# Kernel tuning notes

Hardware: AMD Instinct MI355X
Metric: run time of the kernel (lower is better)

## Reference

```python
import jax, jax.numpy as jnp
import numpy as np


def setup_inputs() -> dict:
    key = jax.random.key(0)
    ks = jax.random.split(key, 5)
    B, H, W, KV = 32, 32, 32, 1024
    N, K, V = 16, 64, 64
    return {
        "key_value": jax.random.normal(ks[0], (B, H, W, KV), dtype=jnp.float32),
        "query": jax.random.normal(ks[1], (1, 1, N, K), dtype=jnp.float32),
        "k_kernel": jax.random.normal(ks[2], (KV, N * K), dtype=jnp.float32) * 0.03,
        "k_bias": jnp.zeros((N * K,), dtype=jnp.float32),
        "v_kernel": jax.random.normal(ks[3], (KV, N * V), dtype=jnp.float32) * 0.03,
        "v_bias": jnp.zeros((N * V,), dtype=jnp.float32),
    }


def reference(key_value, query, k_kernel, k_bias, v_kernel, v_bias):
    # key_value: [B,H,W,KV]; 1x1 conv == channel GEMM
    B, H, W, KV = key_value.shape
    N, K = query.shape[2], query.shape[3]
    V = v_kernel.shape[1] // N
    x = key_value.reshape(B, H * W, KV)                      # [B,HW,KV]
    k = (x @ k_kernel + k_bias).reshape(B, H * W, N, K)       # [B,HW,N,K]
    v = (x @ v_kernel + v_bias).reshape(B, H * W, N, V)       # [B,HW,N,V]
    # single-query dot product per head (no 1/sqrt(K) scaling, per original)
    logits = jnp.einsum('bsnk,nk->bsn', k, query[0, 0])       # [B,HW,N]
    attn = jax.nn.softmax(logits, axis=1)                     # softmax over HW
    out = jnp.einsum('bsn,bsnv->bnv', attn, v)                # [B,N,V]
    return out
```

## Files before the change

### kernel.cpp

```cpp
#include <hip/hip_runtime.h>
#include <hip/hip_fp16.h>


__device__ __forceinline__ float rlane(float v, int l) {
  return __int_as_float(__builtin_amdgcn_readlane(__float_as_int(v), l));
}

__global__ __launch_bounds__(256) void k_qk(const float* __restrict__ kk,
                                            const float* __restrict__ q,
                                            const float* __restrict__ kb,
                                            float* __restrict__ qk2,
                                            float* __restrict__ qb) {
  const int gid = blockIdx.x * 256 + threadIdx.x;
  const int c = gid >> 4, n = gid & 15;
  float a = 0.f;
#pragma unroll
  for (int k4 = 0; k4 < 64; k4 += 4) {
    const float4 kv = *(const float4*)(kk + (size_t)c * 1024 + n * 64 + k4);
    const float4 qv = *(const float4*)(q + n * 64 + k4);
    a += kv.x * qv.x + kv.y * qv.y + kv.z * qv.z + kv.w * qv.w;
  }
  qk2[(n >> 2) * 4096 + c * 4 + (n & 3)] = a;
  if (blockIdx.x == 0 && threadIdx.x < 16) {
    float s = 0.f;
    for (int k = 0; k < 64; k++) s += kb[threadIdx.x * 64 + k] * q[threadIdx.x * 64 + k];
    qb[threadIdx.x] = s;
  }
}

__global__ __launch_bounds__(512, 4) void k_fused(const float* __restrict__ x,
                                                  const float* __restrict__ qk2,
                                                  const float* __restrict__ qb,
                                                  float* __restrict__ mch,
                                                  float* __restrict__ lch,
                                                  __half* __restrict__ wph) {
  __shared__ float qkt[16384];
  __shared__ float et2[64 * 17 + 4];
  const int tid = threadIdx.x;
  const int lane = tid & 63;
  const int wid = tid >> 6;
  const int blk = blockIdx.x;
  const int srow0 = blk * 64;

#pragma unroll
  for (int it = 0; it < 8; ++it) {
    const int g = it * 512 + tid;
    *(float4*)&qkt[g * 4] = *(const float4*)(qk2 + (size_t)g * 4);
  }
  __syncthreads();

#pragma unroll 1
  for (int sweep = 0; sweep < 2; ++sweep) {
    const int rloc = sweep * 32 + wid * 4;
    const float* xw = x + (size_t)(srow0 + rloc) * 1024 + lane;

    float acc[4][16];
#pragma unroll
    for (int r = 0; r < 4; ++r)
#pragma unroll
      for (int n = 0; n < 16; ++n) acc[r][n] = 0.f;

    float xa[4], xb[4];
#pragma unroll
    for (int r = 0; r < 4; ++r) xa[r] = xw[(size_t)r * 1024];

#pragma unroll 1
    for (int st = 0; st < 16; st += 2) {
#pragma unroll
      for (int r = 0; r < 4; ++r) xb[r] = xw[(size_t)r * 1024 + (st + 1) * 64];
      {
        const int c4 = (st * 64 + lane) * 4;
#pragma unroll
        for (int nq = 0; nq < 4; ++nq) {
          const float4 qv = *(const float4*)&qkt[nq * 4096 + c4];
#pragma unroll
          for (int r = 0; r < 4; ++r) {
            acc[r][nq * 4 + 0] += xa[r] * qv.x;
            acc[r][nq * 4 + 1] += xa[r] * qv.y;
            acc[r][nq * 4 + 2] += xa[r] * qv.z;
            acc[r][nq * 4 + 3] += xa[r] * qv.w;
          }
        }
      }
      if (st + 2 < 16) {
#pragma unroll
        for (int r = 0; r < 4; ++r) xa[r] = xw[(size_t)r * 1024 + (st + 2) * 64];
      }
      {
        const int c4 = ((st + 1) * 64 + lane) * 4;
#pragma unroll
        for (int nq = 0; nq < 4; ++nq) {
          const float4 qv = *(const float4*)&qkt[nq * 4096 + c4];
#pragma unroll
          for (int r = 0; r < 4; ++r) {
            acc[r][nq * 4 + 0] += xb[r] * qv.x;
            acc[r][nq * 4 + 1] += xb[r] * qv.y;
            acc[r][nq * 4 + 2] += xb[r] * qv.z;
            acc[r][nq * 4 + 3] += xb[r] * qv.w;
          }
        }
      }
    }

    const int b0 = lane & 1, b1 = (lane >> 1) & 1;
    const int b2 = (lane >> 2) & 1, b3 = (lane >> 3) & 1;
    float f[4];
#pragma unroll
    for (int r = 0; r < 4; ++r) {
      float u[8];
#pragma unroll
      for (int m = 0; m < 8; ++m) {
        const float keep = b0 ? acc[r][2 * m + 1] : acc[r][2 * m];
        const float give = b0 ? acc[r][2 * m]     : acc[r][2 * m + 1];
        u[m] = keep + __shfl_xor(give, 1);
      }
      float w[4];
#pragma unroll
      for (int p = 0; p < 4; ++p) {
        const float keep = b1 ? u[2 * p + 1] : u[2 * p];
        const float give = b1 ? u[2 * p]     : u[2 * p + 1];
        w[p] = keep + __shfl_xor(give, 2);
      }
      float z[2];
#pragma unroll
      for (int qq = 0; qq < 2; ++qq) {
        const float keep = b2 ? w[2 * qq + 1] : w[2 * qq];
        const float give = b2 ? w[2 * qq]     : w[2 * qq + 1];
        z[qq] = keep + __shfl_xor(give, 4);
      }
      {
        const float keep = b3 ? z[1] : z[0];
        const float give = b3 ? z[0] : z[1];
        float t = keep + __shfl_xor(give, 8);
        t += __shfl_xor(t, 16);
        t += __shfl_xor(t, 32);
        f[r] = t;
      }
    }
    const int rsel = lane >> 4;
    float val = (rsel == 0) ? f[0] : (rsel == 1) ? f[1] : (rsel == 2) ? f[2] : f[3];
    val += qb[lane & 15];
    et2[(rloc + rsel) * 17 + (lane & 15)] = val;
  }
  __syncthreads();

#pragma unroll
  for (int t = 0; t < 2; ++t) {
    const int nn = wid + t * 8;
    const float v = et2[lane * 17 + nn];
    float m = v;
#pragma unroll
    for (int d = 1; d < 64; d <<= 1) m = fmaxf(m, __shfl_xor(m, d));
    const float e = __expf(v - m);
    float s = e;
#pragma unroll
    for (int d = 1; d < 64; d <<= 1) s += __shfl_xor(s, d);
    if (lane == 0) {
      mch[blk * 16 + nn] = m;
      lch[blk * 16 + nn] = s;
    }
    et2[lane * 17 + nn] = e;
  }
  __syncthreads();

  {
    const int c0 = tid * 2;
    float acc0[16], acc1[16];
#pragma unroll
    for (int n = 0; n < 16; ++n) { acc0[n] = 0.f; acc1[n] = 0.f; }
    const float* xp = x + (size_t)srow0 * 1024 + c0;

    float  ea = et2[(lane >> 4) * 17 + (lane & 15)];
    float2 xca[4];
#pragma unroll
    for (int ss = 0; ss < 4; ++ss) xca[ss] = *(const float2*)(xp + (size_t)ss * 1024);

#pragma unroll 1
    for (int sg = 0; sg < 16; ++sg) {
      float  eb = 0.f;
      float2 xcb[4];
      if (sg < 15) {
        const int s0n = (sg + 1) * 4;
        eb = et2[(s0n + (lane >> 4)) * 17 + (lane & 15)];
#pragma unroll
        for (int ss = 0; ss < 4; ++ss)
          xcb[ss] = *(const float2*)(xp + (size_t)(s0n + ss) * 1024);
      }
#pragma unroll
      for (int ss = 0; ss < 4; ++ss) {
#pragma unroll
        for (int n = 0; n < 16; ++n) {
          const float ev = rlane(ea, ss * 16 + n);
          acc0[n] += ev * xca[ss].x;
          acc1[n] += ev * xca[ss].y;
        }
      }
      ea = eb;
#pragma unroll
      for (int ss = 0; ss < 4; ++ss) xca[ss] = xcb[ss];
    }

    __half* wpp = wph + (size_t)blk * 16384;
#pragma unroll
    for (int n = 0; n < 16; ++n) {
      __half2 h = __floats2half2_rn(acc0[n], acc1[n]);
      *(__half2*)(wpp + n * 1024 + c0) = h;
    }
  }
}

__global__ __launch_bounds__(256) void k_out(const __half* __restrict__ wph,
                                             const float* __restrict__ vk,
                                             const float* __restrict__ vb,
                                             const float* __restrict__ mch,
                                             const float* __restrict__ lch,
                                             float* __restrict__ out) {
  const int bi = blockIdx.x;
  const int b = bi >> 4, n = bi & 15;
  const int tid = threadIdx.x;
  __shared__ float wrow[1024];
  __shared__ float red[4][64];

  float m16[16], l16[16];
#pragma unroll
  for (int ch = 0; ch < 16; ++ch) {
    m16[ch] = mch[(b * 16 + ch) * 16 + n];
    l16[ch] = lch[(b * 16 + ch) * 16 + n];
  }
  float mg = m16[0];
#pragma unroll
  for (int ch = 1; ch < 16; ++ch) mg = fmaxf(mg, m16[ch]);
  float fac[16], lg = 0.f;
#pragma unroll
  for (int ch = 0; ch < 16; ++ch) { fac[ch] = __expf(m16[ch] - mg); lg += fac[ch] * l16[ch]; }

  float4 a4 = {0.f, 0.f, 0.f, 0.f};
#pragma unroll
  for (int ch = 0; ch < 16; ch++) {
    const __half2* p = (const __half2*)(wph + ((size_t)(b * 16 + ch) * 16 + n) * 1024 + tid * 4);
    const float2 f01 = __half22float2(p[0]);
    const float2 f23 = __half22float2(p[1]);
    a4.x += fac[ch] * f01.x; a4.y += fac[ch] * f01.y;
    a4.z += fac[ch] * f23.x; a4.w += fac[ch] * f23.y;
  }
  *(float4*)&wrow[tid * 4] = a4;
  __syncthreads();

  const int v = tid & 63, cq = tid >> 6;
  float a = 0.f;
  const float* vkc = vk + n * 64 + v;
  for (int ci = 0; ci < 256; ci++) {
    const int c = cq * 256 + ci;
    a += wrow[c] * vkc[(size_t)c * 1024];
  }
  red[cq][v] = a;
  __syncthreads();
  if (tid < 64) {
    const float o = (red[0][tid] + red[1][tid] + red[2][tid] + red[3][tid]) / lg
                    + vb[n * 64 + tid];
    out[(size_t)b * 1024 + n * 64 + tid] = o;
  }
}

extern "C" void kernel_launch(void* const* d_in, const int* in_sizes, int n_in,
                              void* d_out, int out_size, void* d_ws, size_t ws_size,
                              hipStream_t stream) {
  const float* x  = (const float*)d_in[0];
  const float* q  = (const float*)d_in[1];
  const float* kk = (const float*)d_in[2];
  const float* kb = (const float*)d_in[3];
  const float* vk = (const float*)d_in[4];
  const float* vb = (const float*)d_in[5];
  float* out = (float*)d_out;

  float*  f   = (float*)d_ws;
  float*  qk2 = f;
  float*  qb  = f + 16384;
  float*  mch = f + 16400;
  float*  lch = f + 24592;
  __half* wph = (__half*)(f + 32784);

  hipLaunchKernelGGL(k_qk,    dim3(64),  dim3(256), 0, stream, kk, q, kb, qk2, qb);
  hipLaunchKernelGGL(k_fused, dim3(512), dim3(512), 0, stream, x, qk2, qb, mch, lch, wph);
  hipLaunchKernelGGL(k_out,   dim3(512), dim3(256), 0, stream, wph, vk, vb, mch, lch, out);
}
```

Measured before the change: 68.98 us.

## Split fused attention kernel across two head halves per row chunk

The fused logits/softmax/weighted-sum kernel now gives each block 8 heads instead of 16, and the grid doubles to 1024 blocks. The qk table in shared memory is halved and the launch bound raised to 8 blocks per CU, aiming for more parallelism and occupancy. The cost is that each row of x is now read twice, once per head half, which adds global memory traffic. The producer and consumer indexing were updated to match the new head-split layout.

```diff
diff --git a/kernel.cpp b/kernel.cpp
--- a/kernel.cpp
+++ b/kernel.cpp
@@ -20,7 +20,7 @@
     const float4 qv = *(const float4*)(q + n * 64 + k4);
     a += kv.x * qv.x + kv.y * qv.y + kv.z * qv.z + kv.w * qv.w;
   }
-  qk2[(n >> 2) * 4096 + c * 4 + (n & 3)] = a;
+  qk2[(n >> 3) * 8192 + ((n >> 2) & 1) * 4096 + c * 4 + (n & 3)] = a;
   if (blockIdx.x == 0 && threadIdx.x < 16) {
     float s = 0.f;
     for (int k = 0; k < 64; k++) s += kb[threadIdx.x * 64 + k] * q[threadIdx.x * 64 + k];
@@ -28,24 +28,28 @@
   }
 }
 
-__global__ __launch_bounds__(512, 4) void k_fused(const float* __restrict__ x,
+__global__ __launch_bounds__(512, 8) void k_fused(const float* __restrict__ x,
                                                   const float* __restrict__ qk2,
                                                   const float* __restrict__ qb,
                                                   float* __restrict__ mch,
                                                   float* __restrict__ lch,
                                                   __half* __restrict__ wph) {
-  __shared__ float qkt[16384];
-  __shared__ float et2[64 * 17 + 4];
+  __shared__ float qkt[8192];
+  __shared__ float et2[64 * 9 + 4];
   const int tid = threadIdx.x;
   const int lane = tid & 63;
   const int wid = tid >> 6;
   const int blk = blockIdx.x;
-  const int srow0 = blk * 64;
-
-#pragma unroll
-  for (int it = 0; it < 8; ++it) {
-    const int g = it * 512 + tid;
-    *(float4*)&qkt[g * 4] = *(const float4*)(qk2 + (size_t)g * 4);
+  const int nh = blk & 1;
+  const int srow0 = (blk >> 1) * 64;
+
+  {
+    const float* qsrc = qk2 + (size_t)nh * 8192;
+#pragma unroll
+    for (int it = 0; it < 4; ++it) {
+      const int g = it * 512 + tid;
+      *(float4*)&qkt[g * 4] = *(const float4*)(qsrc + (size_t)g * 4);
+    }
   }
   __syncthreads();
 
@@ -54,11 +58,11 @@
     const int rloc = sweep * 32 + wid * 4;
     const float* xw = x + (size_t)(srow0 + rloc) * 1024 + lane;
 
-    float acc[4][16];
+    float acc[4][8];
 #pragma unroll
     for (int r = 0; r < 4; ++r)
 #pragma unroll
-      for (int n = 0; n < 16; ++n) acc[r][n] = 0.f;
+      for (int n = 0; n < 8; ++n) acc[r][n] = 0.f;
 
     float xa[4], xb[4];
 #pragma unroll
@@ -71,7 +75,7 @@
       {
         const int c4 = (st * 64 + lane) * 4;
 #pragma unroll
-        for (int nq = 0; nq < 4; ++nq) {
+        for (int nq = 0; nq < 2; ++nq) {
           const float4 qv = *(const float4*)&qkt[nq * 4096 + c4];
 #pragma unroll
           for (int r = 0; r < 4; ++r) {
@@ -89,7 +93,7 @@
       {
         const int c4 = ((st + 1) * 64 + lane) * 4;
 #pragma unroll
-        for (int nq = 0; nq < 4; ++nq) {
+        for (int nq = 0; nq < 2; ++nq) {
           const float4 qv = *(const float4*)&qkt[nq * 4096 + c4];
 #pragma unroll
           for (int r = 0; r < 4; ++r) {
@@ -102,52 +106,43 @@
       }
     }
 
-    const int b0 = lane & 1, b1 = (lane >> 1) & 1;
-    const int b2 = (lane >> 2) & 1, b3 = (lane >> 3) & 1;
+    const int b0 = lane & 1, b1 = (lane >> 1) & 1, b2 = (lane >> 2) & 1;
     float f[4];
 #pragma unroll
     for (int r = 0; r < 4; ++r) {
-      float u[8];
-#pragma unroll
-      for (int m = 0; m < 8; ++m) {
+      float u[4];
+#pragma unroll
+      for (int m = 0; m < 4; ++m) {
         const float keep = b0 ? acc[r][2 * m + 1] : acc[r][2 * m];
         const float give = b0 ? acc[r][2 * m]     : acc[r][2 * m + 1];
         u[m] = keep + __shfl_xor(give, 1);
       }
-      float w[4];
-#pragma unroll
-      for (int p = 0; p < 4; ++p) {
+      float w[2];
+#pragma unroll
+      for (int p = 0; p < 2; ++p) {
         const float keep = b1 ? u[2 * p + 1] : u[2 * p];
         const float give = b1 ? u[2 * p]     : u[2 * p + 1];
         w[p] = keep + __shfl_xor(give, 2);
       }
-      float z[2];
-#pragma unroll
-      for (int qq = 0; qq < 2; ++qq) {
-        const float keep = b2 ? w[2 * qq + 1] : w[2 * qq];
-        const float give = b2 ? w[2 * qq]     : w[2 * qq + 1];
-        z[qq] = keep + __shfl_xor(give, 4);
-      }
       {
-        const float keep = b3 ? z[1] : z[0];
-        const float give = b3 ? z[0] : z[1];
-        float t = keep + __shfl_xor(give, 8);
+        const float keep = b2 ? w[1] : w[0];
+        const float give = b2 ? w[0] : w[1];
+        float t = keep + __shfl_xor(give, 4);
+        t += __shfl_xor(t, 8);
         t += __shfl_xor(t, 16);
         t += __shfl_xor(t, 32);
         f[r] = t;
       }
     }
-    const int rsel = lane >> 4;
+    const int rsel = (lane >> 3) & 3;
     float val = (rsel == 0) ? f[0] : (rsel == 1) ? f[1] : (rsel == 2) ? f[2] : f[3];
-    val += qb[lane & 15];
-    et2[(rloc + rsel) * 17 + (lane & 15)] = val;
-  }
-  __syncthreads();
-
-#pragma unroll
-  for (int t = 0; t < 2; ++t) {
-    const int nn = wid + t * 8;
-    const float v = et2[lane * 17 + nn];
+    val += qb[nh * 8 + (lane & 7)];
+    if (lane < 32) et2[(rloc + rsel) * 9 + (lane & 7)] = val;
+  }
+  __syncthreads();
+
+  {
+    const float v = et2[lane * 9 + wid];
     float m = v;
 #pragma unroll
     for (int d = 1; d < 64; d <<= 1) m = fmaxf(m, __shfl_xor(m, d));
@@ -156,21 +151,21 @@
 #pragma unroll
     for (int d = 1; d < 64; d <<= 1) s += __shfl_xor(s, d);
     if (lane == 0) {
-      mch[blk * 16 + nn] = m;
-      lch[blk * 16 + nn] = s;
-    }
-    et2[lane * 17 + nn] = e;
+      mch[blk * 8 + wid] = m;
+      lch[blk * 8 + wid] = s;
+    }
+    et2[lane * 9 + wid] = e;
   }
   __syncthreads();
 
   {
     const int c0 = tid * 2;
-    float acc0[16], acc1[16];
-#pragma unroll
-    for (int n = 0; n < 16; ++n) { acc0[n] = 0.f; acc1[n] = 0.f; }
+    float acc0[8], acc1[8];
+#pragma unroll
+    for (int n = 0; n < 8; ++n) { acc0[n] = 0.f; acc1[n] = 0.f; }
     const float* xp = x + (size_t)srow0 * 1024 + c0;
 
-    float  ea = et2[(lane >> 4) * 17 + (lane & 15)];
+    float  ea = et2[((lane >> 3) & 3) * 9 + (lane & 7)];
     float2 xca[4];
 #pragma unroll
     for (int ss = 0; ss < 4; ++ss) xca[ss] = *(const float2*)(xp + (size_t)ss * 1024);
@@ -181,7 +176,7 @@
       float2 xcb[4];
       if (sg < 15) {
         const int s0n = (sg + 1) * 4;
-        eb = et2[(s0n + (lane >> 4)) * 17 + (lane & 15)];
+        eb = et2[(s0n + ((lane >> 3) & 3)) * 9 + (lane & 7)];
 #pragma unroll
         for (int ss = 0; ss < 4; ++ss)
           xcb[ss] = *(const float2*)(xp + (size_t)(s0n + ss) * 1024);
@@ -189,8 +184,8 @@
 #pragma unroll
       for (int ss = 0; ss < 4; ++ss) {
 #pragma unroll
-        for (int n = 0; n < 16; ++n) {
-          const float ev = rlane(ea, ss * 16 + n);
+        for (int n = 0; n < 8; ++n) {
+          const float ev = rlane(ea, ss * 8 + n);
           acc0[n] += ev * xca[ss].x;
           acc1[n] += ev * xca[ss].y;
         }
@@ -200,9 +195,9 @@
       for (int ss = 0; ss < 4; ++ss) xca[ss] = xcb[ss];
     }
 
-    __half* wpp = wph + (size_t)blk * 16384;
-#pragma unroll
-    for (int n = 0; n < 16; ++n) {
+    __half* wpp = wph + (size_t)blk * 8192;
+#pragma unroll
+    for (int n = 0; n < 8; ++n) {
       __half2 h = __floats2half2_rn(acc0[n], acc1[n]);
       *(__half2*)(wpp + n * 1024 + c0) = h;
     }
@@ -217,6 +212,7 @@
                                              float* __restrict__ out) {
   const int bi = blockIdx.x;
   const int b = bi >> 4, n = bi & 15;
+  const int nh = n >> 3, nl = n & 7;
   const int tid = threadIdx.x;
   __shared__ float wrow[1024];
   __shared__ float red[4][64];
@@ -224,8 +220,9 @@
   float m16[16], l16[16];
 #pragma unroll
   for (int ch = 0; ch < 16; ++ch) {
-    m16[ch] = mch[(b * 16 + ch) * 16 + n];
-    l16[ch] = lch[(b * 16 + ch) * 16 + n];
+    const int cblk = ((b * 16 + ch) * 2 + nh);
+    m16[ch] = mch[cblk * 8 + nl];
+    l16[ch] = lch[cblk * 8 + nl];
   }
   float mg = m16[0];
 #pragma unroll
@@ -237,7 +234,8 @@
   float4 a4 = {0.f, 0.f, 0.f, 0.f};
 #pragma unroll
   for (int ch = 0; ch < 16; ch++) {
-    const __half2* p = (const __half2*)(wph + ((size_t)(b * 16 + ch) * 16 + n) * 1024 + tid * 4);
+    const int cblk = ((b * 16 + ch) * 2 + nh);
+    const __half2* p = (const __half2*)(wph + ((size_t)cblk * 8 + nl) * 1024 + tid * 4);
     const float2 f01 = __half22float2(p[0]);
     const float2 f23 = __half22float2(p[1]);
     a4.x += fac[ch] * f01.x; a4.y += fac[ch] * f01.y;
@@ -280,7 +278,7 @@
   float*  lch = f + 24592;
   __half* wph = (__half*)(f + 32784);
 
-  hipLaunchKernelGGL(k_qk,    dim3(64),  dim3(256), 0, stream, kk, q, kb, qk2, qb);
-  hipLaunchKernelGGL(k_fused, dim3(512), dim3(512), 0, stream, x, qk2, qb, mch, lch, wph);
-  hipLaunchKernelGGL(k_out,   dim3(512), dim3(256), 0, stream, wph, vk, vb, mch, lch, out);
-}
+  hipLaunchKernelGGL(k_qk,    dim3(64),   dim3(256), 0, stream, kk, q, kb, qk2, qb);
+  hipLaunchKernelGGL(k_fused, dim3(1024), dim3(512), 0, stream, x, qk2, qb, mch, lch, wph);
+  hipLaunchKernelGGL(k_out,   dim3(512),  dim3(256), 0, stream, wph, vk, vb, mch, lch, out);
+}
```

Measured after the change: 112.1 us. 1.62x slower.
